# Kernel tuning notes

Hardware: AMD Instinct MI355X
Metric: run time of the kernel (lower is better)

Reference implementation:

```python
import jax, jax.numpy as jnp
import numpy as np

N_NODES = 100000
N_EDGES = 1200000


def setup_inputs() -> dict:
    key = jax.random.key(0)
    k1, k2, k3, k4 = jax.random.split(key, 4)
    x = jax.random.normal(k1, (N_NODES, 64), dtype=jnp.float32)
    edge_index = jax.random.randint(k2, (2, N_EDGES), 0, N_NODES, dtype=jnp.int64)
    W1 = jax.random.normal(k3, (64, 64), dtype=jnp.float32) * (1.0 / np.sqrt(64))
    b1 = jnp.zeros((64,), dtype=jnp.float32)
    W2 = jax.random.normal(k4, (64, 32), dtype=jnp.float32) * (1.0 / np.sqrt(64))
    b2 = jnp.zeros((32,), dtype=jnp.float32)
    return {"x": x, "edge_index": edge_index, "W1": W1, "b1": b1, "W2": W2, "b2": b2}


def _gcn_layer(x, src, dst, norm, W, b, n_nodes):
    # x: [N, Fin]; src/dst: [E'] (with self-loops); norm: [E']
    h = x @ W                      # [N, Fout] -- linear transform first (PyG GCNConv)
    msg = h[src] * norm[:, None]   # gather + edge-wise scale, [E', Fout]
    out = jax.ops.segment_sum(msg, dst, num_segments=n_nodes)  # scatter-add
    return out + b


def _gcn_norm(edge_index, n_nodes):
    # add self-loops, then symmetric normalization D^{-1/2} A_hat D^{-1/2}
    loop = jnp.arange(n_nodes, dtype=edge_index.dtype)
    src = jnp.concatenate([edge_index[0], loop])
    dst = jnp.concatenate([edge_index[1], loop])
    ones = jnp.ones(src.shape[0], dtype=jnp.float32)
    deg = jax.ops.segment_sum(ones, dst, num_segments=n_nodes)  # in-degree incl. self-loop
    dinv = jnp.where(deg > 0, jax.lax.rsqrt(deg), 0.0)
    norm = dinv[src] * dinv[dst]
    return src, dst, norm


def reference(x, edge_index, W1, b1, W2, b2):
    n_nodes = x.shape[0]
    src, dst, norm = _gcn_norm(edge_index, n_nodes)
    h = _gcn_layer(x, src, dst, norm, W1, b1, n_nodes)   # op1: GCNConv(in, hidden)
    out = _gcn_layer(h, src, dst, norm, W2, b2, n_nodes) # op2: GCNConv(hidden, out)
    return out
```

## Files before the change

kernel.cpp:

```cpp
#include <hip/hip_runtime.h>


#define TPB 256
#define NPB 512
#define BCAP 8192
#define TILE_E 4096
#define W_ELL 20

typedef __attribute__((ext_vector_type(8))) short bf16x8;
typedef __attribute__((ext_vector_type(4))) float f32x4;

__device__ __forceinline__ float bf2f(unsigned short u) {
    unsigned int v = ((unsigned int)u) << 16;
    return __builtin_bit_cast(float, v);
}
__device__ __forceinline__ unsigned short f2bf(float f) {
    unsigned int u = __builtin_bit_cast(unsigned int, f);
    u += 0x7FFFu + ((u >> 16) & 1u);
    return (unsigned short)(u >> 16);
}
__device__ __forceinline__ int edge_val(const void* ei, int is64, long long idx) {
    if (is64) return (int)((const long long*)ei)[idx];
    return ((const int*)ei)[idx];
}

__global__ void k_detect(const unsigned int* __restrict__ w, int nelems, int* flag,
                         int* __restrict__ bucket_wp, int* __restrict__ ovf_cnt,
                         unsigned short* __restrict__ T0b, unsigned short* __restrict__ T1b,
                         float* __restrict__ dinv, int n_nodes,
                         const float* __restrict__ W1, const float* __restrict__ W2,
                         const float* __restrict__ b1,
                         unsigned short* __restrict__ W12Tb, float* __restrict__ c1) {
    int t = threadIdx.x;
    if (blockIdx.x == 1) {
        __shared__ float W1s[64][64];
        __shared__ float W2s[64][32];
        for (int i = t; i < 4096; i += TPB) W1s[i >> 6][i & 63] = W1[i];
        for (int i = t; i < 2048; i += TPB) W2s[i >> 5][i & 31] = W2[i];
        __syncthreads();
        for (int i = t; i < 2048; i += TPB) {
            int f = i >> 6, k = i & 63;
            float acc = 0.f;
#pragma unroll
            for (int j = 0; j < 64; ++j) acc += W1s[k][j] * W2s[j][f];
            W12Tb[i] = f2bf(acc);
        }
        if (t < 32) {
            float acc = 0.f;
#pragma unroll
            for (int j = 0; j < 64; ++j) acc += b1[j] * W2s[j][t];
            c1[t] = acc;
        }
        return;
    }
    __shared__ unsigned int red[TPB];
    bucket_wp[t] = 0;
    if (t == 0) {
        *ovf_cnt = 0;
        dinv[n_nodes] = 0.f;
    }
    if (t < 32) {
        T0b[(size_t)n_nodes * 32 + t] = 0;
        T1b[(size_t)n_nodes * 32 + t] = 0;
    }
    unsigned int acc = 0;
    int limit = nelems < 16384 ? nelems : 16384;
    for (int i = 1 + 2 * t; i < limit; i += 2 * TPB) acc |= w[i];
    red[t] = acc;
    __syncthreads();
    for (int s = TPB / 2; s > 0; s >>= 1) {
        if (t < s) red[t] |= red[t + s];
        __syncthreads();
    }
    if (t == 0) *flag = (red[0] == 0u) ? 1 : 0;
}

__launch_bounds__(512)
__global__ void k_binA(const void* __restrict__ ei, const int* __restrict__ flag, int E,
                       int nb, unsigned int* __restrict__ gstage, int* __restrict__ bucket_wp) {
    __shared__ int lcnt[256];
    __shared__ int lboff[256];
    __shared__ int lrank[256];
    __shared__ int gbase[256];
    __shared__ int sh[256];
    __shared__ unsigned int spair[TILE_E];
    __shared__ unsigned char sbuck[TILE_E];
    int is64 = *flag;
    int t = threadIdx.x;
    int base_e = blockIdx.x * TILE_E;
    int ne = E - base_e;
    if (ne > TILE_E) ne = TILE_E;

    if (t < 256) {
        lcnt[t] = 0;
        lrank[t] = 0;
    }
    __syncthreads();

    int myb[8];
    unsigned int mypair[8];
#pragma unroll
    for (int k = 0; k < 8; ++k) {
        int idx = t + k * 512;
        myb[k] = -1;
        if (idx < ne) {
            long long e = base_e + idx;
            int s = edge_val(ei, is64, e);
            int d = edge_val(ei, is64, (long long)E + e);
            int b = d >> 9;
            myb[k] = b;
            mypair[k] = (unsigned int)s | ((unsigned int)(d & (NPB - 1)) << 20);
            atomicAdd(&lcnt[b], 1);
        }
    }
    __syncthreads();

    int v0 = (t < 256) ? lcnt[t] : 0;
    if (t < 256) sh[t] = v0;
    __syncthreads();
    for (int st = 1; st < 256; st <<= 1) {
        int u = (t >= st && t < 256) ? sh[t - st] : 0;
        __syncthreads();
        if (t < 256) sh[t] += u;
        __syncthreads();
    }
    if (t < 256) {
        lboff[t] = sh[t] - v0;
        if (t < nb && v0 > 0) gbase[t] = atomicAdd(&bucket_wp[t], v0);
    }
    __syncthreads();

#pragma unroll
    for (int k = 0; k < 8; ++k) {
        int b = myb[k];
        if (b >= 0) {
            int r = atomicAdd(&lrank[b], 1);
            int slot = lboff[b] + r;
            spair[slot] = mypair[k];
            sbuck[slot] = (unsigned char)b;
        }
    }
    __syncthreads();

    for (int j = t; j < ne; j += 512) {
        int b = sbuck[j];
        int pos = gbase[b] + (j - lboff[b]);
        if (pos < BCAP) gstage[(size_t)b * BCAP + pos] = spair[j];
    }
}

__launch_bounds__(512)
__global__ void k_ellB(const unsigned int* __restrict__ gstage, const int* __restrict__ bucket_wp,
                       int* __restrict__ ell, int* __restrict__ cnt, int* __restrict__ ovf,
                       int* __restrict__ ovf_cnt, float* __restrict__ ovfacc1,
                       float* __restrict__ ovfacc2, int n_nodes) {
    __shared__ int lrank[NPB];
    __shared__ int slab[NPB * W_ELL];
    int b = blockIdx.x, t = threadIdx.x;
    int zr = n_nodes;
    lrank[t] = 0;
    {
        int4 z4 = make_int4(zr, zr, zr, zr);
        for (int j = t; j < NPB * W_ELL / 4; j += 512) ((int4*)slab)[j] = z4;
    }
    __syncthreads();
    int cb = bucket_wp[b];
    if (cb > BCAP) cb = BCAP;
    const unsigned int* gp = gstage + (size_t)b * BCAP;
    for (int j = t; j < cb; j += 512) {
        unsigned int w = gp[j];
        int dl = (int)(w >> 20);
        int src = (int)(w & 0xFFFFFu);
        int r = atomicAdd(&lrank[dl], 1);
        if (r < W_ELL) {
            slab[dl * W_ELL + r] = src;
        } else {
            int o = atomicAdd(ovf_cnt, 1);
            ovf[2 * o] = src;
            ovf[2 * o + 1] = b * NPB + dl;
        }
    }
    __syncthreads();
    int node = b * NPB + t;
    if (node < n_nodes) {
        cnt[node] = lrank[t];
        if (lrank[t] > W_ELL) {
            float4 z = make_float4(0.f, 0.f, 0.f, 0.f);
            float4* z1 = (float4*)(ovfacc1 + (size_t)node * 32);
            float4* z2 = (float4*)(ovfacc2 + (size_t)node * 32);
#pragma unroll
            for (int j = 0; j < 8; ++j) {
                z1[j] = z;
                z2[j] = z;
            }
        }
    }
    {
        int4* dst = (int4*)(ell + (size_t)b * (NPB * W_ELL));
        for (int j = t; j < NPB * W_ELL / 4; j += 512) dst[j] = ((int4*)slab)[j];
    }
}

__launch_bounds__(TPB)
__global__ void k_gemm0(const float* __restrict__ x, const unsigned short* __restrict__ W12Tb,
                        const int* __restrict__ cnt, float* __restrict__ dinv,
                        unsigned short* __restrict__ T0b, int n_nodes) {
    int t = threadIdx.x;
    int w = t >> 6, lane = t & 63;
    int r = lane & 15, kb = lane >> 4;
    int nb = (blockIdx.x * 4 + w) * 16;
    if (nb >= n_nodes) return;
    int ar = nb + r;
    if (ar > n_nodes - 1) ar = n_nodes - 1;
    const float* xp = x + (size_t)ar * 64 + kb * 8;
    float4 v0 = ((const float4*)xp)[0];
    float4 v1 = ((const float4*)xp)[1];
    float4 v2 = ((const float4*)(xp + 32))[0];
    float4 v3 = ((const float4*)(xp + 32))[1];
    union { bf16x8 v; unsigned short e[8]; } a0, a1;
    a0.e[0] = f2bf(v0.x); a0.e[1] = f2bf(v0.y); a0.e[2] = f2bf(v0.z); a0.e[3] = f2bf(v0.w);
    a0.e[4] = f2bf(v1.x); a0.e[5] = f2bf(v1.y); a0.e[6] = f2bf(v1.z); a0.e[7] = f2bf(v1.w);
    a1.e[0] = f2bf(v2.x); a1.e[1] = f2bf(v2.y); a1.e[2] = f2bf(v2.z); a1.e[3] = f2bf(v2.w);
    a1.e[4] = f2bf(v3.x); a1.e[5] = f2bf(v3.y); a1.e[6] = f2bf(v3.z); a1.e[7] = f2bf(v3.w);

    int rnode = nb + 4 * kb;
    float d[4];
    bool full = (nb + 16 <= n_nodes);
    if (full) {
        int4 c4 = *(const int4*)(cnt + rnode);
        d[0] = rsqrtf((float)(c4.x + 1));
        d[1] = rsqrtf((float)(c4.y + 1));
        d[2] = rsqrtf((float)(c4.z + 1));
        d[3] = rsqrtf((float)(c4.w + 1));
        if (r == 0) *(float4*)(dinv + rnode) = make_float4(d[0], d[1], d[2], d[3]);
    } else {
#pragma unroll
        for (int j = 0; j < 4; ++j) {
            int n2 = rnode + j;
            d[j] = (n2 < n_nodes) ? rsqrtf((float)(cnt[n2] + 1)) : 0.f;
            if (r == 0 && n2 < n_nodes) dinv[n2] = d[j];
        }
    }

#pragma unroll
    for (int ft = 0; ft < 2; ++ft) {
        const unsigned short* bp = W12Tb + (size_t)(ft * 16 + r) * 64 + kb * 8;
        bf16x8 b0 = *(const bf16x8*)bp;
        bf16x8 b1v = *(const bf16x8*)(bp + 32);
        f32x4 acc = {0.f, 0.f, 0.f, 0.f};
        acc = __builtin_amdgcn_mfma_f32_16x16x32_bf16(a0.v, b0, acc, 0, 0, 0);
        acc = __builtin_amdgcn_mfma_f32_16x16x32_bf16(a1.v, b1v, acc, 0, 0, 0);
#pragma unroll
        for (int j = 0; j < 4; ++j) {
            int n2 = rnode + j;
            if (n2 < n_nodes) T0b[(size_t)n2 * 32 + ft * 16 + r] = f2bf(acc[j] * d[j]);
        }
    }
}

__launch_bounds__(TPB)
__global__ void k_s(const int* __restrict__ ell, const float* __restrict__ dinv,
                    float* __restrict__ sraw, int n_nodes) {
    int t = threadIdx.x;
    int w = t >> 6, lane = t & 63;
    int node = blockIdx.x * 64 + w * 16 + (lane >> 2);
    int j0 = lane & 3;
    if (node >= n_nodes) return;
    const int* ep = ell + (size_t)node * W_ELL;
    float a = dinv[ep[j0]] + dinv[ep[4 + j0]] + dinv[ep[8 + j0]] + dinv[ep[12 + j0]]
            + dinv[ep[16 + j0]];
    a += __shfl_xor(a, 1);
    a += __shfl_xor(a, 2);
    if (j0 == 0) sraw[node] = a + dinv[node];
}

__global__ void k_oflow1(const int* __restrict__ ovf, const int* __restrict__ ovf_cnt,
                         const unsigned short* __restrict__ T0b, const float* __restrict__ dinv,
                         float* __restrict__ ovfacc1, float* __restrict__ sraw) {
    int n = *ovf_cnt;
    int total = n * 8;
    for (int i = blockIdx.x * blockDim.x + threadIdx.x; i < total;
         i += gridDim.x * blockDim.x) {
        int e = i >> 3, fl = i & 7;
        int src = ovf[2 * e], dst = ovf[2 * e + 1];
        ushort4 u = ((const ushort4*)(T0b + (size_t)src * 32))[fl];
        float* hp = ovfacc1 + (size_t)dst * 32 + fl * 4;
        atomicAdd(hp + 0, bf2f(u.x));
        atomicAdd(hp + 1, bf2f(u.y));
        atomicAdd(hp + 2, bf2f(u.z));
        atomicAdd(hp + 3, bf2f(u.w));
        if (fl == 0) atomicAdd(&sraw[dst], dinv[src]);
    }
}

#define GATH32(TBL, S)                                                         \
    {                                                                          \
        ushort4 u = ((const ushort4*)(TBL + (size_t)(S) * 32))[fl];            \
        a0 += bf2f(u.x); a1 += bf2f(u.y); a2 += bf2f(u.z); a3 += bf2f(u.w);    \
    }

__launch_bounds__(TPB)
__global__ void k_agg1(const int* __restrict__ ell, const unsigned short* __restrict__ T0b,
                       const float* __restrict__ dinv, const int* __restrict__ cnt,
                       const float* __restrict__ ovfacc1, unsigned short* __restrict__ T1b,
                       int n_nodes) {
    int t = threadIdx.x;
    int lane = t & 63;
    int g = lane >> 3, fl = lane & 7;
    int node = blockIdx.x * 32 + (t >> 6) * 8 + g;
    if (node >= n_nodes) return;
    int cv = cnt[node];
    const int4* ep = (const int4*)(ell + (size_t)node * W_ELL);
    int4 i0 = ep[0], i1 = ep[1], i2 = ep[2], i3 = ep[3];
    ushort4 su = ((const ushort4*)(T0b + (size_t)node * 32))[fl];
    float a0 = bf2f(su.x), a1 = bf2f(su.y), a2 = bf2f(su.z), a3 = bf2f(su.w);
    GATH32(T0b, i0.x) GATH32(T0b, i0.y) GATH32(T0b, i0.z) GATH32(T0b, i0.w)
    GATH32(T0b, i1.x) GATH32(T0b, i1.y) GATH32(T0b, i1.z) GATH32(T0b, i1.w)
    GATH32(T0b, i2.x) GATH32(T0b, i2.y) GATH32(T0b, i2.z) GATH32(T0b, i2.w)
    GATH32(T0b, i3.x) GATH32(T0b, i3.y) GATH32(T0b, i3.z) GATH32(T0b, i3.w)
    if (__any(cv > 16)) {
        int4 i4 = ep[4];
        GATH32(T0b, i4.x) GATH32(T0b, i4.y) GATH32(T0b, i4.z) GATH32(T0b, i4.w)
    }
    if (cv > W_ELL) {
        float4 ov = ((const float4*)(ovfacc1 + (size_t)node * 32))[fl];
        a0 += ov.x; a1 += ov.y; a2 += ov.z; a3 += ov.w;
    }
    float di = dinv[node];
    float d2 = di * di;
    ushort4 o;
    o.x = f2bf(d2 * a0);
    o.y = f2bf(d2 * a1);
    o.z = f2bf(d2 * a2);
    o.w = f2bf(d2 * a3);
    ((ushort4*)(T1b + (size_t)node * 32))[fl] = o;
}

__global__ void k_oflow2(const int* __restrict__ ovf, const int* __restrict__ ovf_cnt,
                         const unsigned short* __restrict__ T1b, float* __restrict__ ovfacc2) {
    int n = *ovf_cnt;
    int total = n * 8;
    for (int i = blockIdx.x * blockDim.x + threadIdx.x; i < total;
         i += gridDim.x * blockDim.x) {
        int e = i >> 3, fl = i & 7;
        int src = ovf[2 * e], dst = ovf[2 * e + 1];
        ushort4 u = ((const ushort4*)(T1b + (size_t)src * 32))[fl];
        float* hp = ovfacc2 + (size_t)dst * 32 + fl * 4;
        atomicAdd(hp + 0, bf2f(u.x));
        atomicAdd(hp + 1, bf2f(u.y));
        atomicAdd(hp + 2, bf2f(u.z));
        atomicAdd(hp + 3, bf2f(u.w));
    }
}

__launch_bounds__(TPB)
__global__ void k_agg2(const int* __restrict__ ell, const unsigned short* __restrict__ T1b,
                       const float* __restrict__ dinv, const int* __restrict__ cnt,
                       const float* __restrict__ ovfacc2, const float* __restrict__ sraw,
                       const float* __restrict__ c1, const float* __restrict__ b2,
                       float* __restrict__ out, int n_nodes) {
    int t = threadIdx.x;
    int lane = t & 63;
    int g = lane >> 3, fl = lane & 7;
    int node = blockIdx.x * 32 + (t >> 6) * 8 + g;
    if (node >= n_nodes) return;
    int cv = cnt[node];
    const int4* ep = (const int4*)(ell + (size_t)node * W_ELL);
    int4 i0 = ep[0], i1 = ep[1], i2 = ep[2], i3 = ep[3];
    ushort4 su = ((const ushort4*)(T1b + (size_t)node * 32))[fl];
    float a0 = bf2f(su.x), a1 = bf2f(su.y), a2 = bf2f(su.z), a3 = bf2f(su.w);
    GATH32(T1b, i0.x) GATH32(T1b, i0.y) GATH32(T1b, i0.z) GATH32(T1b, i0.w)
    GATH32(T1b, i1.x) GATH32(T1b, i1.y) GATH32(T1b, i1.z) GATH32(T1b, i1.w)
    GATH32(T1b, i2.x) GATH32(T1b, i2.y) GATH32(T1b, i2.z) GATH32(T1b, i2.w)
    GATH32(T1b, i3.x) GATH32(T1b, i3.y) GATH32(T1b, i3.z) GATH32(T1b, i3.w)
    if (__any(cv > 16)) {
        int4 i4 = ep[4];
        GATH32(T1b, i4.x) GATH32(T1b, i4.y) GATH32(T1b, i4.z) GATH32(T1b, i4.w)
    }
    if (cv > W_ELL) {
        float4 ov = ((const float4*)(ovfacc2 + (size_t)node * 32))[fl];
        a0 += ov.x; a1 += ov.y; a2 += ov.z; a3 += ov.w;
    }
    float di = dinv[node];
    float sv = sraw[node];
    float4 cc = ((const float4*)c1)[fl];
    float4 bb = ((const float4*)b2)[fl];
    float4 o;
    o.x = di * (a0 + sv * cc.x) + bb.x;
    o.y = di * (a1 + sv * cc.y) + bb.y;
    o.z = di * (a2 + sv * cc.z) + bb.z;
    o.w = di * (a3 + sv * cc.w) + bb.w;
    ((float4*)(out + (size_t)node * 32))[fl] = o;
}

extern "C" void kernel_launch(void* const* d_in, const int* in_sizes, int n_in,
                              void* d_out, int out_size, void* d_ws, size_t ws_size,
                              hipStream_t stream) {
    const float* x  = (const float*)d_in[0];
    const void*  ei = d_in[1];
    const float* W1 = (const float*)d_in[2];
    const float* b1 = (const float*)d_in[3];
    const float* W2 = (const float*)d_in[4];
    const float* b2 = (const float*)d_in[5];
    float* out = (float*)d_out;

    const int n_nodes = in_sizes[0] / 64;
    const int E = in_sizes[1] / 2;
    const int nb = (n_nodes + NPB - 1) / NPB;

    char* p = (char*)d_ws;
    auto carve = [&](size_t bytes) {
        char* r = p;
        p += (bytes + 255) / 256 * 256;
        return r;
    };
    int* flag      = (int*)carve(sizeof(int));
    int* bucket_wp = (int*)carve(256 * sizeof(int));
    int* ovf_cnt   = (int*)carve(sizeof(int));
    int* cnt       = (int*)carve((size_t)n_nodes * sizeof(int));
    float* dinv    = (float*)carve(((size_t)n_nodes + 1) * sizeof(float));
    float* sraw    = (float*)carve((size_t)n_nodes * sizeof(float));
    unsigned int* gstage = (unsigned int*)carve((size_t)nb * BCAP * sizeof(unsigned int));
    int* ell       = (int*)carve((size_t)nb * NPB * W_ELL * sizeof(int));
    int* ovf       = (int*)carve((size_t)E * 2 * sizeof(int));
    unsigned short* T0b = (unsigned short*)carve(((size_t)n_nodes + 1) * 32 * sizeof(unsigned short));
    unsigned short* T1b = (unsigned short*)carve(((size_t)n_nodes + 1) * 32 * sizeof(unsigned short));
    float* ovfacc1 = (float*)carve((size_t)n_nodes * 32 * sizeof(float));
    float* ovfacc2 = (float*)carve((size_t)n_nodes * 32 * sizeof(float));
    unsigned short* W12Tb = (unsigned short*)carve(32 * 64 * sizeof(unsigned short));
    float* c1      = (float*)carve(32 * sizeof(float));

    k_detect<<<2, TPB, 0, stream>>>((const unsigned int*)ei, in_sizes[1], flag, bucket_wp,
                                    ovf_cnt, T0b, T1b, dinv, n_nodes, W1, W2, b1, W12Tb, c1);
    k_binA<<<(E + TILE_E - 1) / TILE_E, 512, 0, stream>>>(ei, flag, E, nb, gstage, bucket_wp);
    k_ellB<<<nb, 512, 0, stream>>>(gstage, bucket_wp, ell, cnt, ovf, ovf_cnt, ovfacc1,
                                   ovfacc2, n_nodes);
    k_gemm0<<<(n_nodes + 63) / 64, TPB, 0, stream>>>(x, W12Tb, cnt, dinv, T0b, n_nodes);
    k_s<<<(n_nodes + 63) / 64, TPB, 0, stream>>>(ell, dinv, sraw, n_nodes);
    k_oflow1<<<64, TPB, 0, stream>>>(ovf, ovf_cnt, T0b, dinv, ovfacc1, sraw);
    k_agg1<<<(n_nodes + 31) / 32, TPB, 0, stream>>>(ell, T0b, dinv, cnt, ovfacc1, T1b, n_nodes);
    k_oflow2<<<64, TPB, 0, stream>>>(ovf, ovf_cnt, T1b, ovfacc2);
    k_agg2<<<(n_nodes + 31) / 32, TPB, 0, stream>>>(ell, T1b, dinv, cnt, ovfacc2, sraw, c1,
                                                    b2, out, n_nodes);
}
```

Before: 119.2 us.

## Sort ELL rows by degree per block and fuse self-loop sum into agg1

k_ellB now histograms node degrees inside each 512-node block, builds a degree-sorted permutation, and writes ELL rows and per-row counts in sorted order. The aggregation kernels read these so that warps handle nodes of similar degree and can skip gather chunks with wave-uniform checks per four neighbours, cutting wasted gathers of padding entries. The separate k_s kernel is removed: the dinv neighbour sum is computed inside k_agg1, and the overflow contribution to sraw moves to k_oflow2. In exchange the aggregation adds a permutation indirection, output stores become scattered, and the sort adds shared-memory work and extra writes in k_ellB.

```diff
diff --git a/kernel.cpp b/kernel.cpp
--- a/kernel.cpp
+++ b/kernel.cpp
@@ -151,14 +151,18 @@
 
 __launch_bounds__(512)
 __global__ void k_ellB(const unsigned int* __restrict__ gstage, const int* __restrict__ bucket_wp,
-                       int* __restrict__ ell, int* __restrict__ cnt, int* __restrict__ ovf,
-                       int* __restrict__ ovf_cnt, float* __restrict__ ovfacc1,
-                       float* __restrict__ ovfacc2, int n_nodes) {
+                       int* __restrict__ ell, int* __restrict__ cnt, int* __restrict__ perm,
+                       int* __restrict__ cnt_s, int* __restrict__ ovf, int* __restrict__ ovf_cnt,
+                       float* __restrict__ ovfacc1, float* __restrict__ ovfacc2, int n_nodes) {
     __shared__ int lrank[NPB];
     __shared__ int slab[NPB * W_ELL];
+    __shared__ int hist[64];
+    __shared__ int offs[64];
+    __shared__ short sidx[NPB];
     int b = blockIdx.x, t = threadIdx.x;
     int zr = n_nodes;
     lrank[t] = 0;
+    if (t < 64) hist[t] = 0;
     {
         int4 z4 = make_int4(zr, zr, zr, zr);
         for (int j = t; j < NPB * W_ELL / 4; j += 512) ((int4*)slab)[j] = z4;
@@ -182,9 +186,10 @@
     }
     __syncthreads();
     int node = b * NPB + t;
+    int deg = lrank[t];
     if (node < n_nodes) {
-        cnt[node] = lrank[t];
-        if (lrank[t] > W_ELL) {
+        cnt[node] = deg;
+        if (deg > W_ELL) {
             float4 z = make_float4(0.f, 0.f, 0.f, 0.f);
             float4* z1 = (float4*)(ovfacc1 + (size_t)node * 32);
             float4* z2 = (float4*)(ovfacc2 + (size_t)node * 32);
@@ -195,9 +200,38 @@
             }
         }
     }
+    int dcl = deg < 63 ? deg : 63;
+    atomicAdd(&hist[dcl], 1);
+    __syncthreads();
+    if (t < 64) offs[t] = hist[t];
+    __syncthreads();
+    if (t == 0) {
+        int run = 0;
+#pragma unroll
+        for (int j = 0; j < 64; ++j) {
+            int c = offs[j];
+            offs[j] = run;
+            run += c;
+        }
+    }
+    __syncthreads();
+    {
+        int pos = atomicAdd(&offs[dcl], 1);
+        sidx[pos] = (short)t;
+    }
+    __syncthreads();
+    {
+        int l = sidx[t];
+        int gn = b * NPB + l;
+        perm[(size_t)b * NPB + t] = (gn < n_nodes) ? gn : n_nodes;
+        cnt_s[(size_t)b * NPB + t] = lrank[l];
+    }
     {
         int4* dst = (int4*)(ell + (size_t)b * (NPB * W_ELL));
-        for (int j = t; j < NPB * W_ELL / 4; j += 512) dst[j] = ((int4*)slab)[j];
+        for (int j = t; j < NPB * 5; j += 512) {
+            int row = j / 5, part = j - row * 5;
+            dst[j] = *(const int4*)(slab + sidx[row] * W_ELL + part * 4);
+        }
     }
 }
 
@@ -258,25 +292,8 @@
     }
 }
 
-__launch_bounds__(TPB)
-__global__ void k_s(const int* __restrict__ ell, const float* __restrict__ dinv,
-                    float* __restrict__ sraw, int n_nodes) {
-    int t = threadIdx.x;
-    int w = t >> 6, lane = t & 63;
-    int node = blockIdx.x * 64 + w * 16 + (lane >> 2);
-    int j0 = lane & 3;
-    if (node >= n_nodes) return;
-    const int* ep = ell + (size_t)node * W_ELL;
-    float a = dinv[ep[j0]] + dinv[ep[4 + j0]] + dinv[ep[8 + j0]] + dinv[ep[12 + j0]]
-            + dinv[ep[16 + j0]];
-    a += __shfl_xor(a, 1);
-    a += __shfl_xor(a, 2);
-    if (j0 == 0) sraw[node] = a + dinv[node];
-}
-
 __global__ void k_oflow1(const int* __restrict__ ovf, const int* __restrict__ ovf_cnt,
-                         const unsigned short* __restrict__ T0b, const float* __restrict__ dinv,
-                         float* __restrict__ ovfacc1, float* __restrict__ sraw) {
+                         const unsigned short* __restrict__ T0b, float* __restrict__ ovfacc1) {
     int n = *ovf_cnt;
     int total = n * 8;
     for (int i = blockIdx.x * blockDim.x + threadIdx.x; i < total;
@@ -289,7 +306,6 @@
         atomicAdd(hp + 1, bf2f(u.y));
         atomicAdd(hp + 2, bf2f(u.z));
         atomicAdd(hp + 3, bf2f(u.w));
-        if (fl == 0) atomicAdd(&sraw[dst], dinv[src]);
     }
 }
 
@@ -300,24 +316,39 @@
     }
 
 __launch_bounds__(TPB)
-__global__ void k_agg1(const int* __restrict__ ell, const unsigned short* __restrict__ T0b,
-                       const float* __restrict__ dinv, const int* __restrict__ cnt,
-                       const float* __restrict__ ovfacc1, unsigned short* __restrict__ T1b,
+__global__ void k_agg1(const int* __restrict__ ell, const int* __restrict__ perm,
+                       const int* __restrict__ cnt_s, const unsigned short* __restrict__ T0b,
+                       const float* __restrict__ dinv, const float* __restrict__ ovfacc1,
+                       unsigned short* __restrict__ T1b, float* __restrict__ sraw,
                        int n_nodes) {
     int t = threadIdx.x;
     int lane = t & 63;
-    int g = lane >> 3, fl = lane & 7;
-    int node = blockIdx.x * 32 + (t >> 6) * 8 + g;
-    if (node >= n_nodes) return;
-    int cv = cnt[node];
-    const int4* ep = (const int4*)(ell + (size_t)node * W_ELL);
-    int4 i0 = ep[0], i1 = ep[1], i2 = ep[2], i3 = ep[3];
+    int fl = lane & 7;
+    int gidx = blockIdx.x * 32 + (t >> 6) * 8 + (lane >> 3);
+    int node = perm[gidx];
+    int cv = cnt_s[gidx];
+    const int* epi = ell + (size_t)gidx * W_ELL;
+    const int4* ep = (const int4*)epi;
     ushort4 su = ((const ushort4*)(T0b + (size_t)node * 32))[fl];
     float a0 = bf2f(su.x), a1 = bf2f(su.y), a2 = bf2f(su.z), a3 = bf2f(su.w);
-    GATH32(T0b, i0.x) GATH32(T0b, i0.y) GATH32(T0b, i0.z) GATH32(T0b, i0.w)
-    GATH32(T0b, i1.x) GATH32(T0b, i1.y) GATH32(T0b, i1.z) GATH32(T0b, i1.w)
-    GATH32(T0b, i2.x) GATH32(T0b, i2.y) GATH32(T0b, i2.z) GATH32(T0b, i2.w)
-    GATH32(T0b, i3.x) GATH32(T0b, i3.y) GATH32(T0b, i3.z) GATH32(T0b, i3.w)
+    float sv = dinv[epi[fl]] + dinv[epi[8 + fl]];
+    if (fl < 4) sv += dinv[epi[16 + fl]];
+    {
+        int4 i0 = ep[0];
+        GATH32(T0b, i0.x) GATH32(T0b, i0.y) GATH32(T0b, i0.z) GATH32(T0b, i0.w)
+    }
+    if (__any(cv > 4)) {
+        int4 i1 = ep[1];
+        GATH32(T0b, i1.x) GATH32(T0b, i1.y) GATH32(T0b, i1.z) GATH32(T0b, i1.w)
+    }
+    if (__any(cv > 8)) {
+        int4 i2 = ep[2];
+        GATH32(T0b, i2.x) GATH32(T0b, i2.y) GATH32(T0b, i2.z) GATH32(T0b, i2.w)
+    }
+    if (__any(cv > 12)) {
+        int4 i3 = ep[3];
+        GATH32(T0b, i3.x) GATH32(T0b, i3.y) GATH32(T0b, i3.z) GATH32(T0b, i3.w)
+    }
     if (__any(cv > 16)) {
         int4 i4 = ep[4];
         GATH32(T0b, i4.x) GATH32(T0b, i4.y) GATH32(T0b, i4.z) GATH32(T0b, i4.w)
@@ -326,18 +357,25 @@
         float4 ov = ((const float4*)(ovfacc1 + (size_t)node * 32))[fl];
         a0 += ov.x; a1 += ov.y; a2 += ov.z; a3 += ov.w;
     }
-    float di = dinv[node];
-    float d2 = di * di;
-    ushort4 o;
-    o.x = f2bf(d2 * a0);
-    o.y = f2bf(d2 * a1);
-    o.z = f2bf(d2 * a2);
-    o.w = f2bf(d2 * a3);
-    ((ushort4*)(T1b + (size_t)node * 32))[fl] = o;
+    sv += __shfl_xor(sv, 1);
+    sv += __shfl_xor(sv, 2);
+    sv += __shfl_xor(sv, 4);
+    if (node < n_nodes) {
+        float di = dinv[node];
+        float d2 = di * di;
+        ushort4 o;
+        o.x = f2bf(d2 * a0);
+        o.y = f2bf(d2 * a1);
+        o.z = f2bf(d2 * a2);
+        o.w = f2bf(d2 * a3);
+        ((ushort4*)(T1b + (size_t)node * 32))[fl] = o;
+        if (fl == 0) sraw[node] = sv + di;
+    }
 }
 
 __global__ void k_oflow2(const int* __restrict__ ovf, const int* __restrict__ ovf_cnt,
-                         const unsigned short* __restrict__ T1b, float* __restrict__ ovfacc2) {
+                         const unsigned short* __restrict__ T1b, const float* __restrict__ dinv,
+                         float* __restrict__ ovfacc2, float* __restrict__ sraw) {
     int n = *ovf_cnt;
     int total = n * 8;
     for (int i = blockIdx.x * blockDim.x + threadIdx.x; i < total;
@@ -350,46 +388,59 @@
         atomicAdd(hp + 1, bf2f(u.y));
         atomicAdd(hp + 2, bf2f(u.z));
         atomicAdd(hp + 3, bf2f(u.w));
+        if (fl == 0) atomicAdd(&sraw[dst], dinv[src]);
     }
 }
 
 __launch_bounds__(TPB)
-__global__ void k_agg2(const int* __restrict__ ell, const unsigned short* __restrict__ T1b,
-                       const float* __restrict__ dinv, const int* __restrict__ cnt,
-                       const float* __restrict__ ovfacc2, const float* __restrict__ sraw,
-                       const float* __restrict__ c1, const float* __restrict__ b2,
-                       float* __restrict__ out, int n_nodes) {
+__global__ void k_agg2(const int* __restrict__ ell, const int* __restrict__ perm,
+                       const int* __restrict__ cnt_s, const unsigned short* __restrict__ T1b,
+                       const float* __restrict__ dinv, const float* __restrict__ ovfacc2,
+                       const float* __restrict__ sraw, const float* __restrict__ c1,
+                       const float* __restrict__ b2, float* __restrict__ out, int n_nodes) {
     int t = threadIdx.x;
     int lane = t & 63;
-    int g = lane >> 3, fl = lane & 7;
-    int node = blockIdx.x * 32 + (t >> 6) * 8 + g;
-    if (node >= n_nodes) return;
-    int cv = cnt[node];
-    const int4* ep = (const int4*)(ell + (size_t)node * W_ELL);
-    int4 i0 = ep[0], i1 = ep[1], i2 = ep[2], i3 = ep[3];
+    int fl = lane & 7;
+    int gidx = blockIdx.x * 32 + (t >> 6) * 8 + (lane >> 3);
+    int node = perm[gidx];
+    int cv = cnt_s[gidx];
+    const int4* ep = (const int4*)(ell + (size_t)gidx * W_ELL);
     ushort4 su = ((const ushort4*)(T1b + (size_t)node * 32))[fl];
     float a0 = bf2f(su.x), a1 = bf2f(su.y), a2 = bf2f(su.z), a3 = bf2f(su.w);
-    GATH32(T1b, i0.x) GATH32(T1b, i0.y) GATH32(T1b, i0.z) GATH32(T1b, i0.w)
-    GATH32(T1b, i1.x) GATH32(T1b, i1.y) GATH32(T1b, i1.z) GATH32(T1b, i1.w)
-    GATH32(T1b, i2.x) GATH32(T1b, i2.y) GATH32(T1b, i2.z) GATH32(T1b, i2.w)
-    GATH32(T1b, i3.x) GATH32(T1b, i3.y) GATH32(T1b, i3.z) GATH32(T1b, i3.w)
+    {
+        int4 i0 = ep[0];
+        GATH32(T1b, i0.x) GATH32(T1b, i0.y) GATH32(T1b, i0.z) GATH32(T1b, i0.w)
+    }
+    if (__any(cv > 4)) {
+        int4 i1 = ep[1];
+        GATH32(T1b, i1.x) GATH32(T1b, i1.y) GATH32(T1b, i1.z) GATH32(T1b, i1.w)
+    }
+    if (__any(cv > 8)) {
+        int4 i2 = ep[2];
+        GATH32(T1b, i2.x) GATH32(T1b, i2.y) GATH32(T1b, i2.z) GATH32(T1b, i2.w)
+    }
+    if (__any(cv > 12)) {
+        int4 i3 = ep[3];
+        GATH32(T1b, i3.x) GATH32(T1b, i3.y) GATH32(T1b, i3.z) GATH32(T1b, i3.w)
+    }
     if (__any(cv > 16)) {
         int4 i4 = ep[4];
         GATH32(T1b, i4.x) GATH32(T1b, i4.y) GATH32(T1b, i4.z) GATH32(T1b, i4.w)
     }
+    if (node >= n_nodes) return;
     if (cv > W_ELL) {
         float4 ov = ((const float4*)(ovfacc2 + (size_t)node * 32))[fl];
         a0 += ov.x; a1 += ov.y; a2 += ov.z; a3 += ov.w;
     }
     float di = dinv[node];
-    float sv = sraw[node];
+    float svv = sraw[node];
     float4 cc = ((const float4*)c1)[fl];
     float4 bb = ((const float4*)b2)[fl];
     float4 o;
-    o.x = di * (a0 + sv * cc.x) + bb.x;
-    o.y = di * (a1 + sv * cc.y) + bb.y;
-    o.z = di * (a2 + sv * cc.z) + bb.z;
-    o.w = di * (a3 + sv * cc.w) + bb.w;
+    o.x = di * (a0 + svv * cc.x) + bb.x;
+    o.y = di * (a1 + svv * cc.y) + bb.y;
+    o.z = di * (a2 + svv * cc.z) + bb.z;
+    o.w = di * (a3 + svv * cc.w) + bb.w;
     ((float4*)(out + (size_t)node * 32))[fl] = o;
 }
 
@@ -418,6 +469,8 @@
     int* bucket_wp = (int*)carve(256 * sizeof(int));
     int* ovf_cnt   = (int*)carve(sizeof(int));
     int* cnt       = (int*)carve((size_t)n_nodes * sizeof(int));
+    int* perm      = (int*)carve((size_t)nb * NPB * sizeof(int));
+    int* cnt_s     = (int*)carve((size_t)nb * NPB * sizeof(int));
     float* dinv    = (float*)carve(((size_t)n_nodes + 1) * sizeof(float));
     float* sraw    = (float*)carve((size_t)n_nodes * sizeof(float));
     unsigned int* gstage = (unsigned int*)carve((size_t)nb * BCAP * sizeof(unsigned int));
@@ -433,13 +486,13 @@
     k_detect<<<2, TPB, 0, stream>>>((const unsigned int*)ei, in_sizes[1], flag, bucket_wp,
                                     ovf_cnt, T0b, T1b, dinv, n_nodes, W1, W2, b1, W12Tb, c1);
     k_binA<<<(E + TILE_E - 1) / TILE_E, 512, 0, stream>>>(ei, flag, E, nb, gstage, bucket_wp);
-    k_ellB<<<nb, 512, 0, stream>>>(gstage, bucket_wp, ell, cnt, ovf, ovf_cnt, ovfacc1,
-                                   ovfacc2, n_nodes);
+    k_ellB<<<nb, 512, 0, stream>>>(gstage, bucket_wp, ell, cnt, perm, cnt_s, ovf, ovf_cnt,
+                                   ovfacc1, ovfacc2, n_nodes);
     k_gemm0<<<(n_nodes + 63) / 64, TPB, 0, stream>>>(x, W12Tb, cnt, dinv, T0b, n_nodes);
-    k_s<<<(n_nodes + 63) / 64, TPB, 0, stream>>>(ell, dinv, sraw, n_nodes);
-    k_oflow1<<<64, TPB, 0, stream>>>(ovf, ovf_cnt, T0b, dinv, ovfacc1, sraw);
-    k_agg1<<<(n_nodes + 31) / 32, TPB, 0, stream>>>(ell, T0b, dinv, cnt, ovfacc1, T1b, n_nodes);
-    k_oflow2<<<64, TPB, 0, stream>>>(ovf, ovf_cnt, T1b, ovfacc2);
-    k_agg2<<<(n_nodes + 31) / 32, TPB, 0, stream>>>(ell, T1b, dinv, cnt, ovfacc2, sraw, c1,
-                                                    b2, out, n_nodes);
-}
+    k_oflow1<<<64, TPB, 0, stream>>>(ovf, ovf_cnt, T0b, ovfacc1);
+    k_agg1<<<nb * 16, TPB, 0, stream>>>(ell, perm, cnt_s, T0b, dinv, ovfacc1, T1b, sraw,
+                                        n_nodes);
+    k_oflow2<<<64, TPB, 0, stream>>>(ovf, ovf_cnt, T1b, dinv, ovfacc2, sraw);
+    k_agg2<<<nb * 16, TPB, 0, stream>>>(ell, perm, cnt_s, T1b, dinv, ovfacc2, sraw, c1,
+                                        b2, out, n_nodes);
+}
```

After: 128.3 us. +7.7%, slower.
